# Performance work log

Measured on AMD Instinct MI355X. Metric: run time of the kernel, lower is better.

The kernel has to match this reference:

```python
import jax, jax.numpy as jnp
import numpy as np

L_LEVELS = 16
N_FEATS = 2
BASE_RES = 16
LOG2_T = 19
T = 2 ** LOG2_T
BOUND = 1.0
DESIRED_RES = 2048 * BOUND
PER_LEVEL_SCALE = np.exp2(np.log2(DESIRED_RES / BASE_RES) / (L_LEVELS - 1))
PRIMES = np.array([1, 2654435761, 805459861], dtype=np.uint32)
# 8 trilinear corner offsets, [8,3]
OFFSETS = np.array([[(i >> d) & 1 for d in range(3)] for i in range(8)], dtype=np.uint32)


def hash_encode(x, table):
    """x: [N,3] in [-bound,bound]; table: [L, T, F]. Returns [N, L*F]."""
    x01 = jnp.clip((x + BOUND) / (2.0 * BOUND), 0.0, 1.0)  # [N,3]
    feats = []
    for l in range(L_LEVELS):
        scale = BASE_RES * (PER_LEVEL_SCALE ** l) - 1.0  # torch-ngp gridencoder convention
        res = int(np.ceil(scale)) + 1
        pos = x01 * jnp.float32(scale) + 0.5
        pg = jnp.floor(pos)
        frac = pos - pg                                   # [N,3]
        pgi = pg.astype(jnp.uint32)
        corners = pgi[:, None, :] + OFFSETS[None, :, :]   # [N,8,3] uint32
        if res ** 3 <= T:
            # grid small enough: direct (strided) indexing
            r = np.uint32(res)
            idx = corners[..., 0] + corners[..., 1] * r + corners[..., 2] * (r * r)
        else:
            # spatial hash (xor of coord*prime)
            idx = (corners[..., 0] * PRIMES[0]) ^ (corners[..., 1] * PRIMES[1]) ^ (corners[..., 2] * PRIMES[2])
        idx = (idx % np.uint32(T)).astype(jnp.int32)      # [N,8]
        f = table[l][idx]                                 # [N,8,F] gather
        # trilinear weights: prod over dims of frac (if corner bit=1) else 1-frac
        w = jnp.prod(jnp.where(OFFSETS[None, :, :] == 1, frac[:, None, :], 1.0 - frac[:, None, :]), axis=-1)  # [N,8]
        feats.append(jnp.sum(f * w[..., None], axis=1))   # [N,F]
    return jnp.concatenate(feats, axis=-1)                # [N, L*F]


def softplus_beta100(x):
    z = 100.0 * x
    return jnp.where(z > 20.0, x, jnp.log1p(jnp.exp(jnp.minimum(z, 20.0))) / 100.0)


def setup_inputs() -> dict:
    key = jax.random.key(0)
    k = jax.random.split(key, 6)
    N = 1048576
    in_dim = L_LEVELS * N_FEATS  # 32
    hidden = 64
    out_dim = 1 + 15             # sdf + geo_feat
    x = jax.random.uniform(k[0], (N, 3), jnp.float32, -1.0, 1.0)
    table = jax.random.uniform(k[1], (L_LEVELS, T, N_FEATS), jnp.float32, -1e-4, 1e-4)
    W0 = jax.random.normal(k[2], (hidden, in_dim), jnp.float32) * (1.0 / np.sqrt(in_dim))
    b0 = jnp.zeros((hidden,), jnp.float32)
    W1 = jax.random.normal(k[3], (out_dim, hidden), jnp.float32) * (1.0 / np.sqrt(hidden))
    b1 = jnp.zeros((out_dim,), jnp.float32)
    return {"x": x, "table": table, "W0": W0, "b0": b0, "W1": W1, "b1": b1}


def reference(x, table, W0, b0, W1, b1):
    enc = hash_encode(x, table)                      # [N,32]
    h = softplus_beta100(enc @ W0.T + b0)            # [N,64]
    h = h @ W1.T + b1                                # [N,16]
    sdf = h[..., :1]
    geo_feat = h[..., 1:]
    return (sdf, geo_feat)
```

## Files before the change

### kernel.cpp

```cpp
#include <hip/hip_runtime.h>
#include <math.h>

constexpr int      kLevels = 16;
constexpr unsigned kT      = 1u << 19;
constexpr int      kHidden = 64;
constexpr int      kInDim  = 32;
constexpr int      kOutDim = 16;

struct LevelParams {
    float    scale[kLevels];
    unsigned res[kLevels];
    unsigned dense[kLevels];
};

typedef __attribute__((ext_vector_type(8))) short bf16x8;
typedef __attribute__((ext_vector_type(4))) float f32x4;
typedef __attribute__((ext_vector_type(2))) unsigned uint2v;

__device__ inline float bf2f(unsigned short b) {
    unsigned u = ((unsigned)b) << 16;
    return __builtin_bit_cast(float, u);
}
__device__ inline unsigned short f2bf(float f) {
    unsigned u = __builtin_bit_cast(unsigned, f);
    unsigned r = (u + 0x7fffu + ((u >> 16) & 1u)) >> 16;
    return (unsigned short)r;
}
__device__ inline unsigned pack2bf(float a, float b) {
    return (unsigned)f2bf(a) | ((unsigned)f2bf(b) << 16);
}

__global__ __launch_bounds__(256) void convert_table(
        const float* __restrict__ t, unsigned* __restrict__ o, int n4)
{
    int i = blockIdx.x * blockDim.x + threadIdx.x;
    if (i >= n4) return;
    float4 v = ((const float4*)t)[i];
    ((uint2*)o)[i] = make_uint2(pack2bf(v.x, v.y), pack2bf(v.z, v.w));
}

__global__ __launch_bounds__(256) void encode_level(
        const float* __restrict__ x,
        const unsigned* __restrict__ tblAll,
        unsigned* __restrict__ enc,
        int N, int nxb, LevelParams lp)
{
    const int bid = blockIdx.x;
    const int tid = threadIdx.x;

    int l, xb;
    const int pinnedBlocks = 8 * nxb;
    if (bid < pinnedBlocks) {
        l  = 8 + (bid & 7);
        xb = bid >> 3;
    } else {
        const int r = bid - pinnedBlocks;
        l  = r / nxb;
        xb = r - l * nxb;
    }

    const float    scale = lp.scale[l];
    const unsigned res   = lp.res[l];
    const bool     dense = (lp.dense[l] != 0);
    const unsigned* tbl  = tblAll + (size_t)l * kT;

    const int pBase = xb * 1024 + tid;

    float xs[4], ys[4], zs[4];
    #pragma unroll
    for (int q = 0; q < 4; ++q) {
        int p = pBase + q * 256;
        if (p >= N) p = N - 1;
        xs[q] = x[3 * p + 0];
        ys[q] = x[3 * p + 1];
        zs[q] = x[3 * p + 2];
    }

    unsigned v0[4][4], v1[4][4];
    float    wyz[4][4], wgx[4], wfx[4];

    #pragma unroll
    for (int q = 0; q < 4; ++q) {
        const float x0 = fminf(fmaxf((xs[q] + 1.0f) * 0.5f, 0.0f), 1.0f);
        const float y0 = fminf(fmaxf((ys[q] + 1.0f) * 0.5f, 0.0f), 1.0f);
        const float z0 = fminf(fmaxf((zs[q] + 1.0f) * 0.5f, 0.0f), 1.0f);

        const float posx = x0 * scale + 0.5f;
        const float posy = y0 * scale + 0.5f;
        const float posz = z0 * scale + 0.5f;
        const float fgx = floorf(posx), fgy = floorf(posy), fgz = floorf(posz);
        const float fx = posx - fgx, fy = posy - fgy, fz = posz - fgz;
        const float gy = 1.0f - fy,  gz = 1.0f - fz;
        const unsigned ix = (unsigned)fgx, iy = (unsigned)fgy, iz = (unsigned)fgz;

        wgx[q] = 1.0f - fx;
        wfx[q] = fx;

        #pragma unroll
        for (int c2 = 0; c2 < 4; ++c2) {
            const unsigned cy = iy + (c2 & 1);
            const unsigned cz = iz + (c2 >> 1);
            wyz[q][c2] = ((c2 & 1) ? fy : gy) * ((c2 >> 1) ? fz : gz);

            if (dense) {
                const unsigned base = cy * res + cz * res * res;
                const unsigned idx0 = (ix + base) & (kT - 1u);
                if ((idx0 & 1u) == 0u) {
                    const uint2v pr = *(const uint2v*)(tbl + idx0);
                    v0[q][c2] = pr.x; v1[q][c2] = pr.y;
                } else {
                    v0[q][c2] = tbl[idx0];
                    v1[q][c2] = tbl[idx0 + 1u];
                }
            } else {
                const unsigned base = (cy * 2654435761u) ^ (cz * 805459861u);
                const unsigned idx0 = (ix ^ base) & (kT - 1u);
                if ((ix & 1u) == 0u) {
                    const unsigned b = idx0 & ~1u;
                    const uint2v pr = *(const uint2v*)(tbl + b);
                    const bool sw = (idx0 & 1u) != 0u;
                    v0[q][c2] = sw ? pr.y : pr.x;
                    v1[q][c2] = sw ? pr.x : pr.y;
                } else {
                    const unsigned idx1 = ((ix + 1u) ^ base) & (kT - 1u);
                    v0[q][c2] = tbl[idx0];
                    v1[q][c2] = tbl[idx1];
                }
            }
        }
    }

    #pragma unroll
    for (int q = 0; q < 4; ++q) {
        float a0 = 0.0f, a1 = 0.0f;
        #pragma unroll
        for (int c2 = 0; c2 < 4; ++c2) {
            const float w0 = wgx[q] * wyz[q][c2];
            const float w1 = wfx[q] * wyz[q][c2];
            a0 = fmaf(bf2f((unsigned short)(v0[q][c2] & 0xffffu)), w0, a0);
            a1 = fmaf(bf2f((unsigned short)(v0[q][c2] >> 16)),     w0, a1);
            a0 = fmaf(bf2f((unsigned short)(v1[q][c2] & 0xffffu)), w1, a0);
            a1 = fmaf(bf2f((unsigned short)(v1[q][c2] >> 16)),     w1, a1);
        }
        const int p = pBase + q * 256;
        if (p < N)
            __builtin_nontemporal_store(pack2bf(a0, a1), &enc[(size_t)l * N + p]);
    }
}

__global__ __launch_bounds__(256) void mlp_mfma(
        const unsigned* __restrict__ enc,
        const float* __restrict__ W0,
        const float* __restrict__ b0,
        const float* __restrict__ W1,
        const float* __restrict__ b1,
        float* __restrict__ out, int N, int nTiles)
{
    constexpr int kHStride = 72;
    __shared__ short lds_h[4][16 * kHStride];

    const int wave = threadIdx.x >> 6;
    const int lane = threadIdx.x & 63;
    const int quad = lane >> 4;
    const int l16  = lane & 15;

    union Frag { bf16x8 v; short s[8]; unsigned u[4]; };

    Frag w0f[4];
    #pragma unroll
    for (int hb = 0; hb < 4; ++hb) {
        #pragma unroll
        for (int j = 0; j < 8; ++j) {
            const int k = quad * 8 + j;
            const int n = hb * 16 + l16;
            w0f[hb].s[j] = (short)f2bf(W0[n * kInDim + k]);
        }
    }
    Frag w1f[2];
    #pragma unroll
    for (int kb = 0; kb < 2; ++kb) {
        #pragma unroll
        for (int j = 0; j < 8; ++j) {
            const int k = kb * 32 + quad * 8 + j;
            const int n = l16;
            w1f[kb].s[j] = (short)f2bf(W1[n * kHidden + k]);
        }
    }
    float b0v[4];
    #pragma unroll
    for (int hb = 0; hb < 4; ++hb) b0v[hb] = b0[hb * 16 + l16];
    const float b1v = b1[l16];

    short* hrow = lds_h[wave];
    const int waveGlobal = blockIdx.x * 4 + wave;
    const int nWaves     = gridDim.x * 4;

    auto loadFrag = [&](int t, Frag& f) {
        const int P = t * 16;
        int p = P + l16;
        if (p >= N) p = N - 1;
        #pragma unroll
        for (int j2 = 0; j2 < 4; ++j2)
            f.u[j2] = enc[(size_t)(quad * 4 + j2) * N + p];
    };

    int t = waveGlobal;
    if (t >= nTiles) return;

    Frag af;
    loadFrag(t, af);

    for (; t < nTiles; t += nWaves) {
        const int tn = t + nWaves;
        Frag afn;
        if (tn < nTiles) loadFrag(tn, afn);

        const int P = t * 16;

        f32x4 acc[4];
        #pragma unroll
        for (int hb = 0; hb < 4; ++hb) {
            acc[hb] = f32x4{b0v[hb], b0v[hb], b0v[hb], b0v[hb]};
            acc[hb] = __builtin_amdgcn_mfma_f32_16x16x32_bf16(
                          af.v, w0f[hb].v, acc[hb], 0, 0, 0);
        }

        #pragma unroll
        for (int hb = 0; hb < 4; ++hb) {
            #pragma unroll
            for (int r = 0; r < 4; ++r) {
                const float a = acc[hb][r];
                const float z = 100.0f * a;
                const float h = (z > 20.0f) ? a
                              : (__logf(1.0f + __expf(z)) * 0.01f);
                const int row = quad * 4 + r;
                const int col = hb * 16 + l16;
                hrow[row * kHStride + col] = (short)f2bf(h);
            }
        }
        bf16x8 h0 = *(const bf16x8*)&hrow[l16 * kHStride + quad * 8];
        bf16x8 h1 = *(const bf16x8*)&hrow[l16 * kHStride + 32 + quad * 8];

        f32x4 acc2 = f32x4{b1v, b1v, b1v, b1v};
        acc2 = __builtin_amdgcn_mfma_f32_16x16x32_bf16(h0, w1f[0].v, acc2, 0, 0, 0);
        acc2 = __builtin_amdgcn_mfma_f32_16x16x32_bf16(h1, w1f[1].v, acc2, 0, 0, 0);

        #pragma unroll
        for (int r = 0; r < 4; ++r) {
            const int pp = P + quad * 4 + r;
            if (pp < N) {
                if (l16 == 0) out[pp] = acc2[r];
                else out[(size_t)N + (size_t)pp * 15u + (l16 - 1)] = acc2[r];
            }
        }

        af = afn;
    }
}

__global__ __launch_bounds__(256) void sdf_fused(
        const float* __restrict__ x, const float* __restrict__ table,
        const float* __restrict__ W0, const float* __restrict__ b0,
        const float* __restrict__ W1, const float* __restrict__ b1,
        float* __restrict__ out, int N, LevelParams lp)
{
    const int gid = blockIdx.x * blockDim.x + threadIdx.x;
    if (gid >= N) return;
    const float x0 = fminf(fmaxf((x[3 * gid + 0] + 1.0f) * 0.5f, 0.0f), 1.0f);
    const float y0 = fminf(fmaxf((x[3 * gid + 1] + 1.0f) * 0.5f, 0.0f), 1.0f);
    const float z0 = fminf(fmaxf((x[3 * gid + 2] + 1.0f) * 0.5f, 0.0f), 1.0f);
    float enc[kInDim];
    #pragma unroll
    for (int l = 0; l < kLevels; ++l) {
        const float scale = lp.scale[l];
        const unsigned res = lp.res[l];
        const bool dense = (lp.dense[l] != 0);
        const float posx = x0 * scale + 0.5f, posy = y0 * scale + 0.5f, posz = z0 * scale + 0.5f;
        const float fgx = floorf(posx), fgy = floorf(posy), fgz = floorf(posz);
        const float fx = posx - fgx, fy = posy - fgy, fz = posz - fgz;
        const float gx = 1.0f - fx, gy = 1.0f - fy, gz = 1.0f - fz;
        const unsigned ix = (unsigned)fgx, iy = (unsigned)fgy, iz = (unsigned)fgz;
        const float* tbl = table + (size_t)l * kT * 2u;
        float a0 = 0.0f, a1 = 0.0f;
        #pragma unroll
        for (int c = 0; c < 8; ++c) {
            const unsigned cx = ix + (c & 1), cy = iy + ((c >> 1) & 1), cz = iz + ((c >> 2) & 1);
            unsigned idx = dense ? (cx + cy * res + cz * res * res)
                                 : (cx ^ (cy * 2654435761u) ^ (cz * 805459861u));
            idx &= (kT - 1u);
            const float2 tv = *(const float2*)(tbl + 2u * idx);
            const float w = ((c & 1) ? fx : gx) * (((c >> 1) & 1) ? fy : gy) * (((c >> 2) & 1) ? fz : gz);
            a0 = fmaf(tv.x, w, a0); a1 = fmaf(tv.y, w, a1);
        }
        enc[2 * l] = a0; enc[2 * l + 1] = a1;
    }
    float acc[kOutDim];
    #pragma unroll
    for (int k = 0; k < kOutDim; ++k) acc[k] = b1[k];
    #pragma unroll 2
    for (int j = 0; j < kHidden; ++j) {
        float a = b0[j];
        #pragma unroll
        for (int i = 0; i < kInDim; ++i) a = fmaf(enc[i], W0[j * kInDim + i], a);
        const float z = 100.0f * a;
        const float h = (z > 20.0f) ? a : (__logf(1.0f + __expf(z)) * 0.01f);
        #pragma unroll
        for (int k = 0; k < kOutDim; ++k) acc[k] = fmaf(h, W1[k * kHidden + j], acc[k]);
    }
    out[gid] = acc[0];
    #pragma unroll
    for (int k = 0; k < 15; ++k) out[(size_t)N + (size_t)gid * 15u + k] = acc[k + 1];
}

extern "C" void kernel_launch(void* const* d_in, const int* in_sizes, int n_in,
                              void* d_out, int out_size, void* d_ws, size_t ws_size,
                              hipStream_t stream) {
    const float* x     = (const float*)d_in[0];
    const float* table = (const float*)d_in[1];
    const float* W0    = (const float*)d_in[2];
    const float* b0    = (const float*)d_in[3];
    const float* W1    = (const float*)d_in[4];
    const float* b1    = (const float*)d_in[5];
    float* out = (float*)d_out;
    const int N = in_sizes[0] / 3;

    LevelParams lp;
    const double s = exp2(7.0 / 15.0);
    for (int l = 0; l < kLevels; ++l) {
        const double sc = 16.0 * pow(s, (double)l) - 1.0;
        lp.scale[l] = (float)sc;
        const unsigned res = (unsigned)ceil(sc) + 1u;
        lp.res[l] = res;
        lp.dense[l] =
            ((unsigned long long)res * res * res <= (unsigned long long)kT) ? 1u : 0u;
    }

    const size_t tbl_bytes = (size_t)kLevels * kT * 4u;
    const size_t enc_bytes = (size_t)kLevels * (size_t)N * 4u;

    if (ws_size >= tbl_bytes + enc_bytes) {
        unsigned* tbl_bf = (unsigned*)d_ws;
        unsigned* enc    = (unsigned*)((char*)d_ws + tbl_bytes);

        const int n4 = (int)(kLevels * kT * 2u / 4u);
        hipLaunchKernelGGL(convert_table, dim3((n4 + 255) / 256), dim3(256), 0, stream,
                           table, tbl_bf, n4);

        const int nxb = (N + 1023) / 1024;
        hipLaunchKernelGGL(encode_level, dim3(16 * nxb), dim3(256), 0, stream,
                           x, tbl_bf, enc, N, nxb, lp);

        const int nTiles = (N + 15) / 16;
        hipLaunchKernelGGL(mlp_mfma, dim3(2048), dim3(256), 0, stream,
                           enc, W0, b0, W1, b1, out, N, nTiles);
    } else {
        hipLaunchKernelGGL(sdf_fused, dim3((N + 255) / 256), dim3(256), 0, stream,
                           x, table, W0, b0, W1, b1, out, N, lp);
    }
}
```

Baseline: 435.4 us.

## Drop bf16 table conversion pass and gather fp32 table directly

Removes the convert_table kernel that rewrote the whole hash table to bf16 each call, and has encode_level gather float2 entries straight from the fp32 table using float4 paired loads. This saves a full read and write pass over the table (about 64 MB read) but doubles the bytes per gather and the cache footprint of each level's table. It also switches the encoding store from nontemporal to a regular store, so enc is more likely to stay in cache for the MLP, and makes the MLP output stores nontemporal.

```diff
diff --git a/kernel.cpp b/kernel.cpp
--- a/kernel.cpp
+++ b/kernel.cpp
@@ -15,7 +15,6 @@
 
 typedef __attribute__((ext_vector_type(8))) short bf16x8;
 typedef __attribute__((ext_vector_type(4))) float f32x4;
-typedef __attribute__((ext_vector_type(2))) unsigned uint2v;
 
 __device__ inline float bf2f(unsigned short b) {
     unsigned u = ((unsigned)b) << 16;
@@ -30,18 +29,9 @@
     return (unsigned)f2bf(a) | ((unsigned)f2bf(b) << 16);
 }
 
-__global__ __launch_bounds__(256) void convert_table(
-        const float* __restrict__ t, unsigned* __restrict__ o, int n4)
-{
-    int i = blockIdx.x * blockDim.x + threadIdx.x;
-    if (i >= n4) return;
-    float4 v = ((const float4*)t)[i];
-    ((uint2*)o)[i] = make_uint2(pack2bf(v.x, v.y), pack2bf(v.z, v.w));
-}
-
 __global__ __launch_bounds__(256) void encode_level(
         const float* __restrict__ x,
-        const unsigned* __restrict__ tblAll,
+        const float* __restrict__ table,
         unsigned* __restrict__ enc,
         int N, int nxb, LevelParams lp)
 {
@@ -62,7 +52,7 @@
     const float    scale = lp.scale[l];
     const unsigned res   = lp.res[l];
     const bool     dense = (lp.dense[l] != 0);
-    const unsigned* tbl  = tblAll + (size_t)l * kT;
+    const float2*  tbl   = (const float2*)table + (size_t)l * kT;
 
     const int pBase = xb * 1024 + tid;
 
@@ -76,8 +66,8 @@
         zs[q] = x[3 * p + 2];
     }
 
-    unsigned v0[4][4], v1[4][4];
-    float    wyz[4][4], wgx[4], wfx[4];
+    float2 v0[4][4], v1[4][4];
+    float  wyz[4][4], wgx[4], wfx[4];
 
     #pragma unroll
     for (int q = 0; q < 4; ++q) {
@@ -106,8 +96,9 @@
                 const unsigned base = cy * res + cz * res * res;
                 const unsigned idx0 = (ix + base) & (kT - 1u);
                 if ((idx0 & 1u) == 0u) {
-                    const uint2v pr = *(const uint2v*)(tbl + idx0);
-                    v0[q][c2] = pr.x; v1[q][c2] = pr.y;
+                    const float4 pr = *(const float4*)(tbl + idx0);
+                    v0[q][c2] = make_float2(pr.x, pr.y);
+                    v1[q][c2] = make_float2(pr.z, pr.w);
                 } else {
                     v0[q][c2] = tbl[idx0];
                     v1[q][c2] = tbl[idx0 + 1u];
@@ -117,10 +108,10 @@
                 const unsigned idx0 = (ix ^ base) & (kT - 1u);
                 if ((ix & 1u) == 0u) {
                     const unsigned b = idx0 & ~1u;
-                    const uint2v pr = *(const uint2v*)(tbl + b);
+                    const float4 pr = *(const float4*)(tbl + b);
                     const bool sw = (idx0 & 1u) != 0u;
-                    v0[q][c2] = sw ? pr.y : pr.x;
-                    v1[q][c2] = sw ? pr.x : pr.y;
+                    v0[q][c2] = sw ? make_float2(pr.z, pr.w) : make_float2(pr.x, pr.y);
+                    v1[q][c2] = sw ? make_float2(pr.x, pr.y) : make_float2(pr.z, pr.w);
                 } else {
                     const unsigned idx1 = ((ix + 1u) ^ base) & (kT - 1u);
                     v0[q][c2] = tbl[idx0];
@@ -137,14 +128,14 @@
         for (int c2 = 0; c2 < 4; ++c2) {
             const float w0 = wgx[q] * wyz[q][c2];
             const float w1 = wfx[q] * wyz[q][c2];
-            a0 = fmaf(bf2f((unsigned short)(v0[q][c2] & 0xffffu)), w0, a0);
-            a1 = fmaf(bf2f((unsigned short)(v0[q][c2] >> 16)),     w0, a1);
-            a0 = fmaf(bf2f((unsigned short)(v1[q][c2] & 0xffffu)), w1, a0);
-            a1 = fmaf(bf2f((unsigned short)(v1[q][c2] >> 16)),     w1, a1);
+            a0 = fmaf(v0[q][c2].x, w0, a0);
+            a1 = fmaf(v0[q][c2].y, w0, a1);
+            a0 = fmaf(v1[q][c2].x, w1, a0);
+            a1 = fmaf(v1[q][c2].y, w1, a1);
         }
         const int p = pBase + q * 256;
         if (p < N)
-            __builtin_nontemporal_store(pack2bf(a0, a1), &enc[(size_t)l * N + p]);
+            enc[(size_t)l * N + p] = pack2bf(a0, a1);
     }
 }
 
@@ -249,8 +240,11 @@
         for (int r = 0; r < 4; ++r) {
             const int pp = P + quad * 4 + r;
             if (pp < N) {
-                if (l16 == 0) out[pp] = acc2[r];
-                else out[(size_t)N + (size_t)pp * 15u + (l16 - 1)] = acc2[r];
+                if (l16 == 0)
+                    __builtin_nontemporal_store(acc2[r], &out[pp]);
+                else
+                    __builtin_nontemporal_store(acc2[r],
+                        &out[(size_t)N + (size_t)pp * 15u + (l16 - 1)]);
             }
         }
 
@@ -335,20 +329,14 @@
             ((unsigned long long)res * res * res <= (unsigned long long)kT) ? 1u : 0u;
     }
 
-    const size_t tbl_bytes = (size_t)kLevels * kT * 4u;
     const size_t enc_bytes = (size_t)kLevels * (size_t)N * 4u;
 
-    if (ws_size >= tbl_bytes + enc_bytes) {
-        unsigned* tbl_bf = (unsigned*)d_ws;
-        unsigned* enc    = (unsigned*)((char*)d_ws + tbl_bytes);
-
-        const int n4 = (int)(kLevels * kT * 2u / 4u);
-        hipLaunchKernelGGL(convert_table, dim3((n4 + 255) / 256), dim3(256), 0, stream,
-                           table, tbl_bf, n4);
+    if (ws_size >= enc_bytes) {
+        unsigned* enc = (unsigned*)d_ws;
 
         const int nxb = (N + 1023) / 1024;
         hipLaunchKernelGGL(encode_level, dim3(16 * nxb), dim3(256), 0, stream,
-                           x, tbl_bf, enc, N, nxb, lp);
+                           x, table, enc, N, nxb, lp);
 
         const int nTiles = (N + 15) / 16;
         hipLaunchKernelGGL(mlp_mfma, dim3(2048), dim3(256), 0, stream,
```

New measurement: 495.2 us. 1.14x slower.
